# Kernel optimization log

Hardware: AMD Instinct MI355X
Metric: run time of the kernel (lower is better)

Reference implementation:

```python
import jax, jax.numpy as jnp
import numpy as np

VOCAB, EMB_D, HID, NCLS = 50000, 300, 512, 1000
B, T = 64, 512


def setup_inputs() -> dict:
    key = jax.random.key(0)
    ks = jax.random.split(key, 8)
    return {
        "x": jax.random.randint(ks[0], (B, T), 0, VOCAB),
        "emb": jax.random.normal(ks[1], (VOCAB, EMB_D), dtype=jnp.float32),
        "W_ih": jax.random.normal(ks[2], (HID, EMB_D), dtype=jnp.float32) * (1.0 / np.sqrt(HID)),
        "W_hh": jax.random.normal(ks[3], (HID, HID), dtype=jnp.float32) * (1.0 / np.sqrt(HID)),
        "b_ih": jax.random.normal(ks[4], (HID,), dtype=jnp.float32) * 0.01,
        "b_hh": jax.random.normal(ks[5], (HID,), dtype=jnp.float32) * 0.01,
        "W_fc": jax.random.normal(ks[6], (NCLS, HID), dtype=jnp.float32) * (1.0 / np.sqrt(HID)),
        "b_fc": jax.random.normal(ks[7], (NCLS,), dtype=jnp.float32) * 0.01,
    }


def reference(x, emb, W_ih, W_hh, b_ih, b_hh, W_fc, b_fc):
    # Embedding lookup: [B, T, EMB_D]
    xe = emb[x]
    # Precompute input projection for all timesteps (batched GEMM): [B, T, HID]
    xp = jnp.einsum('btd,hd->bth', xe, W_ih) + b_ih
    h0 = jnp.zeros((x.shape[0], W_hh.shape[0]), dtype=xp.dtype)

    def step(h, xt):  # xt: [B, HID]
        h = jnp.tanh(xt + h @ W_hh.T + b_hh)
        return h, None

    # Scan over time; only the final hidden state is needed (out[:, -1, :]).
    hT, _ = jax.lax.scan(step, h0, jnp.swapaxes(xp, 0, 1))
    # Final linear head: [B, NCLS]
    return hT @ W_fc.T + b_fc
```

## Files before the change

### kernel.cpp

```cpp
#include <hip/hip_runtime.h>
#include <hip/hip_bf16.h>

#define T_STEPS 512
#define HID 512
#define EMB_D 300
#define BATCH 64
#define NCLS 1000

typedef __attribute__((ext_vector_type(4))) float f32x4;
typedef __attribute__((ext_vector_type(8))) short bf16x8;
typedef __attribute__((ext_vector_type(4))) unsigned int u32x4;
typedef __attribute__((ext_vector_type(2))) unsigned int u32x2;

union FragU { u32x4 u; bf16x8 b; };

__device__ __forceinline__ unsigned cvtpk(float lo, float hi) {
  unsigned r;
  asm("v_cvt_pk_bf16_f32 %0, %1, %2" : "=v"(r) : "v"(lo), "v"(hi));
  return r;
}

__device__ __forceinline__ bf16x8 pack8(f32x4 lo, f32x4 hi) {
  FragU u;
  u.u = (u32x4){cvtpk(lo.x, lo.y), cvtpk(lo.z, lo.w), cvtpk(hi.x, hi.y), cvtpk(hi.z, hi.w)};
  return u.b;
}

__device__ __forceinline__ float tanh_fast(float x) {
  x = fminf(15.0f, fmaxf(-15.0f, x));
  float e = __builtin_amdgcn_exp2f(x * 2.8853900817779268f);
  return (e - 1.0f) * __builtin_amdgcn_rcpf(e + 1.0f);
}

__device__ __forceinline__ float bf16lo(unsigned u) { return __uint_as_float(u << 16); }
__device__ __forceinline__ float bf16hi(unsigned u) { return __uint_as_float(u & 0xffff0000u); }

#define MFMA16(A, B, C) __builtin_amdgcn_mfma_f32_16x16x32_bf16(A, B, C, 0, 0, 0)

__global__ __launch_bounds__(256) void k0_pack(const float* __restrict__ Whh,
                                               unsigned short* __restrict__ wpack) {
  const int idx = blockIdx.x * 256 + threadIdx.x;
  const int lane = idx & 63;
  const int kk = (idx >> 6) & 15;
  const int tw = (idx >> 10) & 3;
  const int wv = idx >> 12;
  const int c = lane & 15, g = lane >> 4;
  const int i = wv * 64 + tw * 16 + c;
  const int j = kk * 32 + g * 8;
  f32x4 lo = *(const f32x4*)(Whh + (size_t)i * HID + j);
  f32x4 hi = *(const f32x4*)(Whh + (size_t)i * HID + j + 4);
  *(bf16x8*)(wpack + (size_t)idx * 8) = pack8(lo, hi);
}

__global__ __launch_bounds__(256) void k1_embed_proj(
    const int* __restrict__ x, const float* __restrict__ emb,
    const float* __restrict__ Wih, const float* __restrict__ bih,
    const float* __restrict__ bhh, unsigned short* __restrict__ xp) {
  __shared__ unsigned short xe[64][328];
  __shared__ int xi[64];
  const int tid = threadIdx.x;
  const int t = blockIdx.x;
  if (tid < 64) xi[tid] = x[tid * T_STEPS + t];
  __syncthreads();
  {
    const int r = tid >> 2, q = tid & 3;
    const float* src = emb + (size_t)xi[r] * EMB_D;
    for (int jp = q; jp < 150; jp += 4) {
      const int j = jp * 2;
      *(unsigned*)&xe[r][j] = cvtpk(src[j], src[j + 1]);
    }
    if (q == 3) {
      #pragma unroll
      for (int j = 300; j < 328; j += 2) *(unsigned*)&xe[r][j] = 0;
    }
  }
  __syncthreads();

  const int wv = tid >> 6, lane = tid & 63;
  const int c = lane & 15, g = lane >> 4;
  const f32x4 z4 = {0, 0, 0, 0};

  bf16x8 af[4][10];
  #pragma unroll
  for (int a = 0; a < 4; ++a) {
    #pragma unroll
    for (int kk = 0; kk < 10; ++kk)
      af[a][kk] = *(const bf16x8*)&xe[a * 16 + c][kk * 32 + g * 8];
  }

  #pragma unroll 1
  for (int nt8 = 0; nt8 < 8; ++nt8) {
    const int nt = wv * 8 + nt8;
    const int n = nt * 16 + c;
    f32x4 a0 = z4, a1 = z4, a2 = z4, a3 = z4;
    #pragma unroll
    for (int kk = 0; kk < 10; ++kk) {
      const int k0 = kk * 32 + g * 8;
      f32x4 blo = (k0 < EMB_D) ? *(const f32x4*)(Wih + (size_t)n * EMB_D + k0) : z4;
      f32x4 bhi = (k0 + 4 < EMB_D) ? *(const f32x4*)(Wih + (size_t)n * EMB_D + k0 + 4) : z4;
      bf16x8 wfrag = pack8(blo, bhi);
      a0 = MFMA16(wfrag, af[0][kk], a0);
      a1 = MFMA16(wfrag, af[1][kk], a1);
      a2 = MFMA16(wfrag, af[2][kk], a2);
      a3 = MFMA16(wfrag, af[3][kk], a3);
    }
    const int n0 = nt * 16 + g * 4;
    f32x4 bias4 = *(const f32x4*)(bih + n0) + *(const f32x4*)(bhh + n0);
    #pragma unroll
    for (int a = 0; a < 4; ++a) {
      f32x4 o = ((a == 0) ? a0 : (a == 1) ? a1 : (a == 2) ? a2 : a3) + bias4;
      u32x2 pk = {cvtpk(o.x, o.y), cvtpk(o.z, o.w)};
      *(u32x2*)(xp + ((((size_t)t * 4 + a) * 32 + nt) * 64 + lane) * 4) = pk;
    }
  }
}

__global__ __launch_bounds__(512) void k2_rnn(
    const unsigned short* __restrict__ wpack,
    const unsigned short* __restrict__ xp, float* __restrict__ hT) {
  __shared__ unsigned short hbuf[2][16][520];
  __shared__ unsigned short wlds[8][15][512];

  const int tid = threadIdx.x;
  const int wv = tid >> 6, lane = tid & 63;
  const int c = lane & 15, g = lane >> 4;
  const int wg = blockIdx.x;
  const int n_wave = wv * 64;

  const unsigned short* wp = wpack + (size_t)wv * 64 * 512 + (size_t)lane * 8;
  bf16x8 wr0[16], wr1[16], wr2[16], w30;
  #pragma unroll
  for (int kk = 0; kk < 16; ++kk) {
    wr0[kk] = *(const bf16x8*)(wp + (size_t)kk * 512);
    wr1[kk] = *(const bf16x8*)(wp + (size_t)(16 + kk) * 512);
    wr2[kk] = *(const bf16x8*)(wp + (size_t)(32 + kk) * 512);
  }
  w30 = *(const bf16x8*)(wp + (size_t)48 * 512);
  #pragma unroll
  for (int kk = 1; kk < 16; ++kk) {
    bf16x8 f = *(const bf16x8*)(wp + (size_t)(48 + kk) * 512);
    *(bf16x8*)&wlds[wv][kk - 1][lane * 8] = f;
  }

  for (int i = tid; i < 2 * 16 * 520; i += 512) ((unsigned short*)hbuf)[i] = 0;
  __syncthreads();

  const unsigned short* xpb =
      xp + (((size_t)0 * 4 + wg) * 32 + wv * 4) * 256 + (size_t)lane * 4;
  const size_t xstride = (size_t)4 * 32 * 256;
  u32x2 xq0 = *(const u32x2*)(xpb);
  u32x2 xq1 = *(const u32x2*)(xpb + 256);
  u32x2 xq2 = *(const u32x2*)(xpb + 512);
  u32x2 xq3 = *(const u32x2*)(xpb + 768);

  int cur = 0;

  #pragma unroll 1
  for (int t = 0; t < T_STEPS; ++t) {
    f32x4 acc0 = {0,0,0,0}, acc1 = {0,0,0,0}, acc2 = {0,0,0,0}, acc3 = {0,0,0,0};
    const unsigned short* hb = &hbuf[cur][0][0];

    bf16x8 afc = *(const bf16x8*)(hb + c * 520 + g * 8);
    bf16x8 w3c = w30;
    #pragma unroll
    for (int kk = 0; kk < 16; ++kk) {
      bf16x8 afn = afc, w3n = w3c;
      if (kk < 15) {
        afn = *(const bf16x8*)(hb + c * 520 + (kk + 1) * 32 + g * 8);
        w3n = *(const bf16x8*)&wlds[wv][kk][lane * 8];
      }
      acc0 = MFMA16(wr0[kk], afc, acc0);
      acc1 = MFMA16(wr1[kk], afc, acc1);
      acc2 = MFMA16(wr2[kk], afc, acc2);
      acc3 = MFMA16(w3c, afc, acc3);
      afc = afn; w3c = w3n;
    }

    unsigned short* hw = &hbuf[cur ^ 1][c][0];
    #pragma unroll
    for (int tau = 0; tau < 4; ++tau) {
      f32x4 a = (tau == 0) ? acc0 : (tau == 1) ? acc1 : (tau == 2) ? acc2 : acc3;
      u32x2 xq = (tau == 0) ? xq0 : (tau == 1) ? xq1 : (tau == 2) ? xq2 : xq3;
      float t0 = tanh_fast(a.x + bf16lo(xq.x));
      float t1 = tanh_fast(a.y + bf16hi(xq.x));
      float t2 = tanh_fast(a.z + bf16lo(xq.y));
      float t3 = tanh_fast(a.w + bf16hi(xq.y));
      u32x2 hv = {cvtpk(t0, t1), cvtpk(t2, t3)};
      *(u32x2*)(hw + n_wave + tau * 16 + g * 4) = hv;
    }

    if (t + 1 < T_STEPS) {
      const unsigned short* nx = xpb + (size_t)(t + 1) * xstride;
      xq0 = *(const u32x2*)(nx);
      xq1 = *(const u32x2*)(nx + 256);
      xq2 = *(const u32x2*)(nx + 512);
      xq3 = *(const u32x2*)(nx + 768);
    }
    __syncthreads();
    cur ^= 1;
  }

  for (int i = tid; i < 16 * HID; i += 512) {
    const int row = i >> 9, n = i & (HID - 1);
    hT[(size_t)(wg * 16 + row) * HID + n] =
        __uint_as_float((unsigned)hbuf[cur][row][n] << 16);
  }
}

__global__ __launch_bounds__(256) void k3_head(
    const float* __restrict__ hT, const float* __restrict__ Wfc,
    const float* __restrict__ bfc, float* __restrict__ out) {
  __shared__ float hrow[HID];
  const int b = blockIdx.x, tid = threadIdx.x;
  hrow[tid] = hT[(size_t)b * HID + tid];
  hrow[tid + 256] = hT[(size_t)b * HID + tid + 256];
  __syncthreads();
  for (int cc = tid; cc < NCLS; cc += 256) {
    const f32x4* W4 = (const f32x4*)(Wfc + (size_t)cc * HID);
    float s0 = 0, s1 = 0, s2 = 0, s3 = 0;
    #pragma unroll 4
    for (int j = 0; j < HID / 4; ++j) {
      f32x4 w = W4[j];
      f32x4 h4 = *(const f32x4*)(hrow + j * 4);
      s0 += h4.x * w.x; s1 += h4.y * w.y; s2 += h4.z * w.z; s3 += h4.w * w.w;
    }
    out[(size_t)b * NCLS + cc] = bfc[cc] + s0 + s1 + s2 + s3;
  }
}

extern "C" void kernel_launch(void* const* d_in, const int* in_sizes, int n_in,
                              void* d_out, int out_size, void* d_ws, size_t ws_size,
                              hipStream_t stream) {
  (void)in_sizes; (void)n_in; (void)out_size; (void)ws_size;
  const int*   x   = (const int*)d_in[0];
  const float* emb = (const float*)d_in[1];
  const float* Wih = (const float*)d_in[2];
  const float* Whh = (const float*)d_in[3];
  const float* bih = (const float*)d_in[4];
  const float* bhh = (const float*)d_in[5];
  const float* Wfc = (const float*)d_in[6];
  const float* bfc = (const float*)d_in[7];
  float* out = (float*)d_out;

  unsigned short* xp = (unsigned short*)d_ws;
  float* hT = (float*)((char*)d_ws + (size_t)T_STEPS * HID * BATCH * 2);
  unsigned short* wpack = (unsigned short*)((char*)d_ws + (size_t)T_STEPS * HID * BATCH * 2 + (size_t)BATCH * HID * 4);

  k0_pack<<<128, 256, 0, stream>>>(Whh, wpack);
  k1_embed_proj<<<512, 256, 0, stream>>>(x, emb, Wih, bih, bhh, xp);
  k2_rnn<<<4, 512, 0, stream>>>(wpack, xp, hT);
  k3_head<<<64, 256, 0, stream>>>(hT, Wfc, bfc, out);
}
```

Baseline: 969.2 us.

## Fuse embedding projection and RNN recurrence with per-timestep flag handoff

Merges the embedding/input-projection kernel and the recurrent kernel into one launch. Projection blocks publish a per-timestep flag, and the four RNN blocks spin on that flag, so the recurrence can start while later timesteps are still being projected. The RNN part now keeps all four W_hh tiles in registers instead of partly in LDS, and stores h in an MFMA-fragment layout so A fragments load directly. It also interleaves the tanh of one accumulator with the remaining MFMAs and drops the clamp from tanh. Risks: the flags are never reset between calls, so later calls may read xp before it is rewritten. Spin waits also depend on co-residency and on the initial contents of the workspace.

```diff
diff --git a/kernel.cpp b/kernel.cpp
--- a/kernel.cpp
+++ b/kernel.cpp
@@ -27,9 +27,8 @@
 }
 
 __device__ __forceinline__ float tanh_fast(float x) {
-  x = fminf(15.0f, fmaxf(-15.0f, x));
   float e = __builtin_amdgcn_exp2f(x * 2.8853900817779268f);
-  return (e - 1.0f) * __builtin_amdgcn_rcpf(e + 1.0f);
+  return fmaf(-2.0f, __builtin_amdgcn_rcpf(e + 1.0f), 1.0f);
 }
 
 __device__ __forceinline__ float bf16lo(unsigned u) { return __uint_as_float(u << 16); }
@@ -52,158 +51,164 @@
   *(bf16x8*)(wpack + (size_t)idx * 8) = pack8(lo, hi);
 }
 
-__global__ __launch_bounds__(256) void k1_embed_proj(
+__global__ __launch_bounds__(512, 2) void k12_fused(
     const int* __restrict__ x, const float* __restrict__ emb,
     const float* __restrict__ Wih, const float* __restrict__ bih,
-    const float* __restrict__ bhh, unsigned short* __restrict__ xp) {
-  __shared__ unsigned short xe[64][328];
-  __shared__ int xi[64];
+    const float* __restrict__ bhh, unsigned short* __restrict__ xp,
+    const unsigned short* __restrict__ wpack, float* __restrict__ hT,
+    unsigned* flags, int rnn_blocks, int spin) {
+  __shared__ __align__(16) char SM[42240];
   const int tid = threadIdx.x;
-  const int t = blockIdx.x;
-  if (tid < 64) xi[tid] = x[tid * T_STEPS + t];
-  __syncthreads();
-  {
-    const int r = tid >> 2, q = tid & 3;
-    const float* src = emb + (size_t)xi[r] * EMB_D;
-    for (int jp = q; jp < 150; jp += 4) {
-      const int j = jp * 2;
-      *(unsigned*)&xe[r][j] = cvtpk(src[j], src[j + 1]);
-    }
-    if (q == 3) {
-      #pragma unroll
-      for (int j = 300; j < 328; j += 2) *(unsigned*)&xe[r][j] = 0;
-    }
-  }
-  __syncthreads();
-
-  const int wv = tid >> 6, lane = tid & 63;
-  const int c = lane & 15, g = lane >> 4;
-  const f32x4 z4 = {0, 0, 0, 0};
-
-  bf16x8 af[4][10];
-  #pragma unroll
-  for (int a = 0; a < 4; ++a) {
+
+  if ((int)blockIdx.x < rnn_blocks) {
+    const int wg = blockIdx.x;
+    const int wv = tid >> 6, lane = tid & 63;
+    const int c = lane & 15, g = lane >> 4;
+    unsigned short* hfrag = (unsigned short*)SM;
+
+    const unsigned short* wp = wpack + (size_t)wv * 32768 + (size_t)lane * 8;
+    bf16x8 wr0[16], wr1[16], wr2[16], wr3[16];
     #pragma unroll
-    for (int kk = 0; kk < 10; ++kk)
-      af[a][kk] = *(const bf16x8*)&xe[a * 16 + c][kk * 32 + g * 8];
-  }
-
-  #pragma unroll 1
-  for (int nt8 = 0; nt8 < 8; ++nt8) {
-    const int nt = wv * 8 + nt8;
-    const int n = nt * 16 + c;
-    f32x4 a0 = z4, a1 = z4, a2 = z4, a3 = z4;
-    #pragma unroll
-    for (int kk = 0; kk < 10; ++kk) {
-      const int k0 = kk * 32 + g * 8;
-      f32x4 blo = (k0 < EMB_D) ? *(const f32x4*)(Wih + (size_t)n * EMB_D + k0) : z4;
-      f32x4 bhi = (k0 + 4 < EMB_D) ? *(const f32x4*)(Wih + (size_t)n * EMB_D + k0 + 4) : z4;
-      bf16x8 wfrag = pack8(blo, bhi);
-      a0 = MFMA16(wfrag, af[0][kk], a0);
-      a1 = MFMA16(wfrag, af[1][kk], a1);
-      a2 = MFMA16(wfrag, af[2][kk], a2);
-      a3 = MFMA16(wfrag, af[3][kk], a3);
-    }
-    const int n0 = nt * 16 + g * 4;
-    f32x4 bias4 = *(const f32x4*)(bih + n0) + *(const f32x4*)(bhh + n0);
+    for (int kk = 0; kk < 16; ++kk) {
+      wr0[kk] = *(const bf16x8*)(wp + (size_t)kk * 512);
+      wr1[kk] = *(const bf16x8*)(wp + (size_t)(16 + kk) * 512);
+      wr2[kk] = *(const bf16x8*)(wp + (size_t)(32 + kk) * 512);
+      wr3[kk] = *(const bf16x8*)(wp + (size_t)(48 + kk) * 512);
+    }
+
+    for (int i = tid; i < 8192; i += 512) ((unsigned*)hfrag)[i] = 0;
+    __syncthreads();
+
+    const unsigned short* xpb = xp + (size_t)wg * 8192 + (size_t)wv * 1024 + (size_t)lane * 4;
+    const int kkw = wv * 2;
+
+    unsigned fn = 1u;
+    if (spin) fn = __hip_atomic_load(&flags[0], __ATOMIC_ACQUIRE, __HIP_MEMORY_SCOPE_AGENT);
+    int cur = 0;
+
+    #pragma unroll 1
+    for (int t = 0; t < T_STEPS; ++t) {
+      if (spin) {
+        while (fn != 1u)
+          fn = __hip_atomic_load(&flags[t], __ATOMIC_ACQUIRE, __HIP_MEMORY_SCOPE_AGENT);
+      }
+      const unsigned short* xq_p = xpb + (size_t)t * 32768;
+      u32x2 xq0 = *(const u32x2*)(xq_p);
+      u32x2 xq1 = *(const u32x2*)(xq_p + 256);
+      u32x2 xq2 = *(const u32x2*)(xq_p + 512);
+      u32x2 xq3 = *(const u32x2*)(xq_p + 768);
+
+      const unsigned short* hc = hfrag + cur * 8192;
+      bf16x8 af[16];
+      #pragma unroll
+      for (int kk = 0; kk < 16; ++kk)
+        af[kk] = *(const bf16x8*)(hc + kk * 512 + lane * 8);
+
+      if (spin)
+        fn = (t + 1 < T_STEPS)
+                 ? __hip_atomic_load(&flags[t + 1], __ATOMIC_ACQUIRE, __HIP_MEMORY_SCOPE_AGENT)
+                 : 1u;
+
+      f32x4 acc0 = {0,0,0,0}, acc1 = {0,0,0,0}, acc2 = {0,0,0,0}, acc3 = {0,0,0,0};
+      #pragma unroll
+      for (int kk = 0; kk < 16; ++kk) {
+        acc0 = MFMA16(wr0[kk], af[kk], acc0);
+        acc1 = MFMA16(wr1[kk], af[kk], acc1);
+      }
+
+      unsigned short* hn = hfrag + (cur ^ 1) * 8192;
+      auto tanhw = [&](int tau, const f32x4& a, const u32x2& xq) {
+        float t0 = tanh_fast(a.x + bf16lo(xq.x));
+        float t1 = tanh_fast(a.y + bf16hi(xq.x));
+        float t2 = tanh_fast(a.z + bf16lo(xq.y));
+        float t3 = tanh_fast(a.w + bf16hi(xq.y));
+        u32x2 hv = {cvtpk(t0, t1), cvtpk(t2, t3)};
+        *(u32x2*)(hn + (kkw + (tau >> 1)) * 512 +
+                  ((((tau & 1) << 1) + (g >> 1)) * 16 + c) * 8 + ((g & 1) << 2)) = hv;
+      };
+
+      tanhw(0, acc0, xq0);
+      #pragma unroll
+      for (int kk = 0; kk < 16; ++kk) {
+        acc2 = MFMA16(wr2[kk], af[kk], acc2);
+        acc3 = MFMA16(wr3[kk], af[kk], acc3);
+      }
+      tanhw(1, acc1, xq1);
+      tanhw(2, acc2, xq2);
+      tanhw(3, acc3, xq3);
+
+      __syncthreads();
+      cur ^= 1;
+    }
+
+    const unsigned short* hc = hfrag + cur * 8192;
+    for (int i = tid; i < 16 * HID; i += 512) {
+      const int b = i >> 9, n = i & 511;
+      unsigned short v = hc[(n >> 5) * 512 + (((n >> 3) & 3) * 16 + b) * 8 + (n & 7)];
+      hT[(size_t)(wg * 16 + b) * HID + n] = __uint_as_float((unsigned)v << 16);
+    }
+  } else {
+    const int t = blockIdx.x - rnn_blocks;
+    int* xi = (int*)SM;
+    unsigned short (*xe)[328] = (unsigned short (*)[328])(SM + 256);
+    if (tid < 64) xi[tid] = x[tid * T_STEPS + t];
+    __syncthreads();
+    {
+      const int r = tid >> 3, q = tid & 7;
+      const float* src = emb + (size_t)xi[r] * EMB_D;
+      for (int jp = q; jp < 150; jp += 8) {
+        const int j = jp * 2;
+        *(unsigned*)&xe[r][j] = cvtpk(src[j], src[j + 1]);
+      }
+      if (q == 6) { for (int j = 300; j < 314; j += 2) *(unsigned*)&xe[r][j] = 0; }
+      if (q == 7) { for (int j = 314; j < 328; j += 2) *(unsigned*)&xe[r][j] = 0; }
+    }
+    __syncthreads();
+
+    const int wv = tid >> 6, lane = tid & 63;
+    const int c = lane & 15, g = lane >> 4;
+    const f32x4 z4 = {0, 0, 0, 0};
+
+    bf16x8 af[4][10];
     #pragma unroll
     for (int a = 0; a < 4; ++a) {
-      f32x4 o = ((a == 0) ? a0 : (a == 1) ? a1 : (a == 2) ? a2 : a3) + bias4;
-      u32x2 pk = {cvtpk(o.x, o.y), cvtpk(o.z, o.w)};
-      *(u32x2*)(xp + ((((size_t)t * 4 + a) * 32 + nt) * 64 + lane) * 4) = pk;
-    }
-  }
-}
-
-__global__ __launch_bounds__(512) void k2_rnn(
-    const unsigned short* __restrict__ wpack,
-    const unsigned short* __restrict__ xp, float* __restrict__ hT) {
-  __shared__ unsigned short hbuf[2][16][520];
-  __shared__ unsigned short wlds[8][15][512];
-
-  const int tid = threadIdx.x;
-  const int wv = tid >> 6, lane = tid & 63;
-  const int c = lane & 15, g = lane >> 4;
-  const int wg = blockIdx.x;
-  const int n_wave = wv * 64;
-
-  const unsigned short* wp = wpack + (size_t)wv * 64 * 512 + (size_t)lane * 8;
-  bf16x8 wr0[16], wr1[16], wr2[16], w30;
-  #pragma unroll
-  for (int kk = 0; kk < 16; ++kk) {
-    wr0[kk] = *(const bf16x8*)(wp + (size_t)kk * 512);
-    wr1[kk] = *(const bf16x8*)(wp + (size_t)(16 + kk) * 512);
-    wr2[kk] = *(const bf16x8*)(wp + (size_t)(32 + kk) * 512);
-  }
-  w30 = *(const bf16x8*)(wp + (size_t)48 * 512);
-  #pragma unroll
-  for (int kk = 1; kk < 16; ++kk) {
-    bf16x8 f = *(const bf16x8*)(wp + (size_t)(48 + kk) * 512);
-    *(bf16x8*)&wlds[wv][kk - 1][lane * 8] = f;
-  }
-
-  for (int i = tid; i < 2 * 16 * 520; i += 512) ((unsigned short*)hbuf)[i] = 0;
-  __syncthreads();
-
-  const unsigned short* xpb =
-      xp + (((size_t)0 * 4 + wg) * 32 + wv * 4) * 256 + (size_t)lane * 4;
-  const size_t xstride = (size_t)4 * 32 * 256;
-  u32x2 xq0 = *(const u32x2*)(xpb);
-  u32x2 xq1 = *(const u32x2*)(xpb + 256);
-  u32x2 xq2 = *(const u32x2*)(xpb + 512);
-  u32x2 xq3 = *(const u32x2*)(xpb + 768);
-
-  int cur = 0;
-
-  #pragma unroll 1
-  for (int t = 0; t < T_STEPS; ++t) {
-    f32x4 acc0 = {0,0,0,0}, acc1 = {0,0,0,0}, acc2 = {0,0,0,0}, acc3 = {0,0,0,0};
-    const unsigned short* hb = &hbuf[cur][0][0];
-
-    bf16x8 afc = *(const bf16x8*)(hb + c * 520 + g * 8);
-    bf16x8 w3c = w30;
-    #pragma unroll
-    for (int kk = 0; kk < 16; ++kk) {
-      bf16x8 afn = afc, w3n = w3c;
-      if (kk < 15) {
-        afn = *(const bf16x8*)(hb + c * 520 + (kk + 1) * 32 + g * 8);
-        w3n = *(const bf16x8*)&wlds[wv][kk][lane * 8];
-      }
-      acc0 = MFMA16(wr0[kk], afc, acc0);
-      acc1 = MFMA16(wr1[kk], afc, acc1);
-      acc2 = MFMA16(wr2[kk], afc, acc2);
-      acc3 = MFMA16(w3c, afc, acc3);
-      afc = afn; w3c = w3n;
-    }
-
-    unsigned short* hw = &hbuf[cur ^ 1][c][0];
-    #pragma unroll
-    for (int tau = 0; tau < 4; ++tau) {
-      f32x4 a = (tau == 0) ? acc0 : (tau == 1) ? acc1 : (tau == 2) ? acc2 : acc3;
-      u32x2 xq = (tau == 0) ? xq0 : (tau == 1) ? xq1 : (tau == 2) ? xq2 : xq3;
-      float t0 = tanh_fast(a.x + bf16lo(xq.x));
-      float t1 = tanh_fast(a.y + bf16hi(xq.x));
-      float t2 = tanh_fast(a.z + bf16lo(xq.y));
-      float t3 = tanh_fast(a.w + bf16hi(xq.y));
-      u32x2 hv = {cvtpk(t0, t1), cvtpk(t2, t3)};
-      *(u32x2*)(hw + n_wave + tau * 16 + g * 4) = hv;
-    }
-
-    if (t + 1 < T_STEPS) {
-      const unsigned short* nx = xpb + (size_t)(t + 1) * xstride;
-      xq0 = *(const u32x2*)(nx);
-      xq1 = *(const u32x2*)(nx + 256);
-      xq2 = *(const u32x2*)(nx + 512);
-      xq3 = *(const u32x2*)(nx + 768);
-    }
-    __syncthreads();
-    cur ^= 1;
-  }
-
-  for (int i = tid; i < 16 * HID; i += 512) {
-    const int row = i >> 9, n = i & (HID - 1);
-    hT[(size_t)(wg * 16 + row) * HID + n] =
-        __uint_as_float((unsigned)hbuf[cur][row][n] << 16);
+      #pragma unroll
+      for (int kk = 0; kk < 10; ++kk)
+        af[a][kk] = *(const bf16x8*)&xe[a * 16 + c][kk * 32 + g * 8];
+    }
+
+    #pragma unroll 1
+    for (int nt4 = 0; nt4 < 4; ++nt4) {
+      const int nt = wv * 4 + nt4;
+      const int n = nt * 16 + c;
+      f32x4 a0 = z4, a1 = z4, a2 = z4, a3 = z4;
+      #pragma unroll
+      for (int kk = 0; kk < 10; ++kk) {
+        const int k0 = kk * 32 + g * 8;
+        f32x4 blo = (k0 < EMB_D) ? *(const f32x4*)(Wih + (size_t)n * EMB_D + k0) : z4;
+        f32x4 bhi = (k0 + 4 < EMB_D) ? *(const f32x4*)(Wih + (size_t)n * EMB_D + k0 + 4) : z4;
+        bf16x8 wf = pack8(blo, bhi);
+        a0 = MFMA16(wf, af[0][kk], a0);
+        a1 = MFMA16(wf, af[1][kk], a1);
+        a2 = MFMA16(wf, af[2][kk], a2);
+        a3 = MFMA16(wf, af[3][kk], a3);
+      }
+      const int n0 = nt * 16 + g * 4;
+      f32x4 bias4 = *(const f32x4*)(bih + n0) + *(const f32x4*)(bhh + n0);
+      #pragma unroll
+      for (int a = 0; a < 4; ++a) {
+        f32x4 o = ((a == 0) ? a0 : (a == 1) ? a1 : (a == 2) ? a2 : a3) + bias4;
+        u32x2 pk = {cvtpk(o.x, o.y), cvtpk(o.z, o.w)};
+        *(u32x2*)(xp + (((size_t)t * 4 + a) * 32 + nt) * 256 + lane * 4) = pk;
+      }
+    }
+    if (flags) {
+      __syncthreads();
+      if (tid == 0) {
+        __threadfence();
+        __hip_atomic_store(&flags[t], 1u, __ATOMIC_RELEASE, __HIP_MEMORY_SCOPE_AGENT);
+      }
+    }
   }
 }
 
@@ -231,7 +236,7 @@
 extern "C" void kernel_launch(void* const* d_in, const int* in_sizes, int n_in,
                               void* d_out, int out_size, void* d_ws, size_t ws_size,
                               hipStream_t stream) {
-  (void)in_sizes; (void)n_in; (void)out_size; (void)ws_size;
+  (void)in_sizes; (void)n_in; (void)out_size;
   const int*   x   = (const int*)d_in[0];
   const float* emb = (const float*)d_in[1];
   const float* Wih = (const float*)d_in[2];
@@ -242,12 +247,24 @@
   const float* bfc = (const float*)d_in[7];
   float* out = (float*)d_out;
 
+  const size_t XP_B = (size_t)T_STEPS * HID * BATCH * 2;
+  const size_t HT_B = (size_t)BATCH * HID * 4;
+  const size_t WP_B = 524288;
   unsigned short* xp = (unsigned short*)d_ws;
-  float* hT = (float*)((char*)d_ws + (size_t)T_STEPS * HID * BATCH * 2);
-  unsigned short* wpack = (unsigned short*)((char*)d_ws + (size_t)T_STEPS * HID * BATCH * 2 + (size_t)BATCH * HID * 4);
+  float* hT = (float*)((char*)d_ws + XP_B);
+  unsigned short* wpack = (unsigned short*)((char*)d_ws + XP_B + HT_B);
+  unsigned* flags = (unsigned*)((char*)d_ws + XP_B + HT_B + WP_B);
+  const bool fused = ws_size >= XP_B + HT_B + WP_B + T_STEPS * sizeof(unsigned);
 
   k0_pack<<<128, 256, 0, stream>>>(Whh, wpack);
-  k1_embed_proj<<<512, 256, 0, stream>>>(x, emb, Wih, bih, bhh, xp);
-  k2_rnn<<<4, 512, 0, stream>>>(wpack, xp, hT);
+  if (fused) {
+    k12_fused<<<4 + T_STEPS, 512, 0, stream>>>(x, emb, Wih, bih, bhh, xp, wpack,
+                                               hT, flags, 4, 1);
+  } else {
+    k12_fused<<<T_STEPS, 512, 0, stream>>>(x, emb, Wih, bih, bhh, xp, wpack,
+                                           hT, nullptr, 0, 0);
+    k12_fused<<<4, 512, 0, stream>>>(x, emb, Wih, bih, bhh, xp, wpack,
+                                     hT, nullptr, 4, 0);
+  }
   k3_head<<<64, 256, 0, stream>>>(hT, Wfc, bfc, out);
 }
```

After: 3.700 ms. +281.8%, slower.

## Store RNN hidden state in MFMA fragment layout and overlap tanh with MFMAs

Applied to the files above, without the earlier changes.

The recurrent kernel now keeps the hidden state in shared memory already arranged in the MFMA B-fragment layout, so each wave loads all 16 K-fragments with contiguous conflict-free 16-byte reads at the start of a step. The step's MFMAs are split into two halves, with the tanh and writeback of the first tile issued between them so the transcendental work overlaps matrix-core execution. tanh is also rewritten as 1 - 2/(e+1) without the clamp, which saves a few ALU ops but depends on exp2 and rcp saturating correctly for large inputs. Holding 16 more fragment registers per step raises register pressure.

```diff
diff --git a/kernel.cpp b/kernel.cpp
--- a/kernel.cpp
+++ b/kernel.cpp
@@ -27,9 +27,8 @@
 }
 
 __device__ __forceinline__ float tanh_fast(float x) {
-  x = fminf(15.0f, fmaxf(-15.0f, x));
   float e = __builtin_amdgcn_exp2f(x * 2.8853900817779268f);
-  return (e - 1.0f) * __builtin_amdgcn_rcpf(e + 1.0f);
+  return fmaf(-2.0f, __builtin_amdgcn_rcpf(e + 1.0f), 1.0f);
 }
 
 __device__ __forceinline__ float bf16lo(unsigned u) { return __uint_as_float(u << 16); }
@@ -98,11 +97,11 @@
       const int k0 = kk * 32 + g * 8;
       f32x4 blo = (k0 < EMB_D) ? *(const f32x4*)(Wih + (size_t)n * EMB_D + k0) : z4;
       f32x4 bhi = (k0 + 4 < EMB_D) ? *(const f32x4*)(Wih + (size_t)n * EMB_D + k0 + 4) : z4;
-      bf16x8 wfrag = pack8(blo, bhi);
-      a0 = MFMA16(wfrag, af[0][kk], a0);
-      a1 = MFMA16(wfrag, af[1][kk], a1);
-      a2 = MFMA16(wfrag, af[2][kk], a2);
-      a3 = MFMA16(wfrag, af[3][kk], a3);
+      bf16x8 wf = pack8(blo, bhi);
+      a0 = MFMA16(wf, af[0][kk], a0);
+      a1 = MFMA16(wf, af[1][kk], a1);
+      a2 = MFMA16(wf, af[2][kk], a2);
+      a3 = MFMA16(wf, af[3][kk], a3);
     }
     const int n0 = nt * 16 + g * 4;
     f32x4 bias4 = *(const f32x4*)(bih + n0) + *(const f32x4*)(bhh + n0);
@@ -110,7 +109,7 @@
     for (int a = 0; a < 4; ++a) {
       f32x4 o = ((a == 0) ? a0 : (a == 1) ? a1 : (a == 2) ? a2 : a3) + bias4;
       u32x2 pk = {cvtpk(o.x, o.y), cvtpk(o.z, o.w)};
-      *(u32x2*)(xp + ((((size_t)t * 4 + a) * 32 + nt) * 64 + lane) * 4) = pk;
+      *(u32x2*)(xp + (((size_t)t * 4 + a) * 32 + nt) * 256 + lane * 4) = pk;
     }
   }
 }
@@ -118,16 +117,15 @@
 __global__ __launch_bounds__(512) void k2_rnn(
     const unsigned short* __restrict__ wpack,
     const unsigned short* __restrict__ xp, float* __restrict__ hT) {
-  __shared__ unsigned short hbuf[2][16][520];
+  __shared__ unsigned short hfrag[2][16][64][8];
   __shared__ unsigned short wlds[8][15][512];
 
   const int tid = threadIdx.x;
   const int wv = tid >> 6, lane = tid & 63;
   const int c = lane & 15, g = lane >> 4;
   const int wg = blockIdx.x;
-  const int n_wave = wv * 64;
-
-  const unsigned short* wp = wpack + (size_t)wv * 64 * 512 + (size_t)lane * 8;
+
+  const unsigned short* wp = wpack + (size_t)wv * 32768 + (size_t)lane * 8;
   bf16x8 wr0[16], wr1[16], wr2[16], w30;
   #pragma unroll
   for (int kk = 0; kk < 16; ++kk) {
@@ -142,55 +140,61 @@
     *(bf16x8*)&wlds[wv][kk - 1][lane * 8] = f;
   }
 
-  for (int i = tid; i < 2 * 16 * 520; i += 512) ((unsigned short*)hbuf)[i] = 0;
-  __syncthreads();
-
-  const unsigned short* xpb =
-      xp + (((size_t)0 * 4 + wg) * 32 + wv * 4) * 256 + (size_t)lane * 4;
-  const size_t xstride = (size_t)4 * 32 * 256;
+  for (int i = tid; i < 8192; i += 512) ((unsigned*)hfrag)[i] = 0;
+  __syncthreads();
+
+  const unsigned short* xpb = xp + (size_t)wg * 8192 + (size_t)wv * 1024 + (size_t)lane * 4;
   u32x2 xq0 = *(const u32x2*)(xpb);
   u32x2 xq1 = *(const u32x2*)(xpb + 256);
   u32x2 xq2 = *(const u32x2*)(xpb + 512);
   u32x2 xq3 = *(const u32x2*)(xpb + 768);
 
+  const int kkw = wv * 2;
   int cur = 0;
 
   #pragma unroll 1
   for (int t = 0; t < T_STEPS; ++t) {
+    const unsigned short* hc = &hfrag[cur][0][0][0];
+    bf16x8 af[16];
+    #pragma unroll
+    for (int kk = 0; kk < 16; ++kk)
+      af[kk] = *(const bf16x8*)(hc + kk * 512 + lane * 8);
+
     f32x4 acc0 = {0,0,0,0}, acc1 = {0,0,0,0}, acc2 = {0,0,0,0}, acc3 = {0,0,0,0};
-    const unsigned short* hb = &hbuf[cur][0][0];
-
-    bf16x8 afc = *(const bf16x8*)(hb + c * 520 + g * 8);
-    bf16x8 w3c = w30;
     #pragma unroll
     for (int kk = 0; kk < 16; ++kk) {
-      bf16x8 afn = afc, w3n = w3c;
-      if (kk < 15) {
-        afn = *(const bf16x8*)(hb + c * 520 + (kk + 1) * 32 + g * 8);
-        w3n = *(const bf16x8*)&wlds[wv][kk][lane * 8];
-      }
-      acc0 = MFMA16(wr0[kk], afc, acc0);
-      acc1 = MFMA16(wr1[kk], afc, acc1);
-      acc2 = MFMA16(wr2[kk], afc, acc2);
-      acc3 = MFMA16(w3c, afc, acc3);
-      afc = afn; w3c = w3n;
-    }
-
-    unsigned short* hw = &hbuf[cur ^ 1][c][0];
-    #pragma unroll
-    for (int tau = 0; tau < 4; ++tau) {
-      f32x4 a = (tau == 0) ? acc0 : (tau == 1) ? acc1 : (tau == 2) ? acc2 : acc3;
-      u32x2 xq = (tau == 0) ? xq0 : (tau == 1) ? xq1 : (tau == 2) ? xq2 : xq3;
+      acc0 = MFMA16(wr0[kk], af[kk], acc0);
+      acc1 = MFMA16(wr1[kk], af[kk], acc1);
+    }
+
+    unsigned short* hn = &hfrag[cur ^ 1][0][0][0];
+    auto tanhw = [&](int tau, const f32x4& a, const u32x2& xq) {
       float t0 = tanh_fast(a.x + bf16lo(xq.x));
       float t1 = tanh_fast(a.y + bf16hi(xq.x));
       float t2 = tanh_fast(a.z + bf16lo(xq.y));
       float t3 = tanh_fast(a.w + bf16hi(xq.y));
       u32x2 hv = {cvtpk(t0, t1), cvtpk(t2, t3)};
-      *(u32x2*)(hw + n_wave + tau * 16 + g * 4) = hv;
-    }
+      *(u32x2*)(hn + (kkw + (tau >> 1)) * 512 +
+                ((((tau & 1) << 1) + (g >> 1)) * 16 + c) * 8 + ((g & 1) << 2)) = hv;
+    };
+
+    tanhw(0, acc0, xq0);
+
+    bf16x8 w3c = w30;
+    #pragma unroll
+    for (int kk = 0; kk < 16; ++kk) {
+      bf16x8 w3n = w3c;
+      if (kk < 15) w3n = *(const bf16x8*)&wlds[wv][kk][lane * 8];
+      acc2 = MFMA16(wr2[kk], af[kk], acc2);
+      acc3 = MFMA16(w3c, af[kk], acc3);
+      w3c = w3n;
+    }
+    tanhw(1, acc1, xq1);
+    tanhw(2, acc2, xq2);
+    tanhw(3, acc3, xq3);
 
     if (t + 1 < T_STEPS) {
-      const unsigned short* nx = xpb + (size_t)(t + 1) * xstride;
+      const unsigned short* nx = xpb + (size_t)(t + 1) * 32768;
       xq0 = *(const u32x2*)(nx);
       xq1 = *(const u32x2*)(nx + 256);
       xq2 = *(const u32x2*)(nx + 512);
@@ -200,10 +204,11 @@
     cur ^= 1;
   }
 
+  const unsigned short* hc = &hfrag[cur][0][0][0];
   for (int i = tid; i < 16 * HID; i += 512) {
-    const int row = i >> 9, n = i & (HID - 1);
-    hT[(size_t)(wg * 16 + row) * HID + n] =
-        __uint_as_float((unsigned)hbuf[cur][row][n] << 16);
+    const int b = i >> 9, n = i & 511;
+    unsigned short v = hc[(n >> 5) * 512 + (((n >> 3) & 3) * 16 + b) * 8 + (n & 7)];
+    hT[(size_t)(wg * 16 + b) * HID + n] = __uint_as_float((unsigned)v << 16);
   }
 }
 
@@ -242,9 +247,11 @@
   const float* bfc = (const float*)d_in[7];
   float* out = (float*)d_out;
 
+  const size_t XP_B = (size_t)T_STEPS * HID * BATCH * 2;
+  const size_t HT_B = (size_t)BATCH * HID * 4;
   unsigned short* xp = (unsigned short*)d_ws;
-  float* hT = (float*)((char*)d_ws + (size_t)T_STEPS * HID * BATCH * 2);
-  unsigned short* wpack = (unsigned short*)((char*)d_ws + (size_t)T_STEPS * HID * BATCH * 2 + (size_t)BATCH * HID * 4);
+  float* hT = (float*)((char*)d_ws + XP_B);
+  unsigned short* wpack = (unsigned short*)((char*)d_ws + XP_B + HT_B);
 
   k0_pack<<<128, 256, 0, stream>>>(Whh, wpack);
   k1_embed_proj<<<512, 256, 0, stream>>>(x, emb, Wih, bih, bhh, xp);
```

New measurement: 1.267 ms. +30.7%, slower.
